# Kernel optimization log

Hardware: AMD Instinct MI355X
Metric: run time of the kernel (lower is better)

The kernel has to match this reference:

```python
import jax, jax.numpy as jnp
import numpy as np

C_IN = 256
GROUP = C_IN // 4  # module hard-codes group = C_in/4 -> 4 channels per group
EPS = 1e-5

@jax.custom_vjp
def binarize(x):
    # 1-bit quantization: sign forward, hardtanh straight-through backward
    return jnp.sign(x)

def _bin_fwd(x):
    return jnp.sign(x), x

def _bin_bwd(x, g):
    return (g * (jnp.abs(x) <= 1.0).astype(g.dtype),)

binarize.defvjp(_bin_fwd, _bin_bwd)

def channel_shuffle(x, g):
    # [N,C,H,W] -> [N,g,C/g,H,W] -> [N,C/g,g,H,W] -> [N,C,H,W]
    N, C, H, W = x.shape
    return x.reshape(N, g, C // g, H, W).transpose(0, 2, 1, 3, 4).reshape(N, C, H, W)


def setup_inputs() -> dict:
    key = jax.random.key(0)
    ks = jax.random.split(key, 6)
    x = jax.random.normal(ks[0], (32, C_IN, 56, 56), jnp.float32)
    # grouped conv weight: [C_out, C_in/group, kH, kW] = [256, 4, 3, 3]
    weight = jax.random.normal(ks[1], (C_IN, C_IN // GROUP, 3, 3), jnp.float32) * 0.1
    gamma = 1.0 + 0.1 * jax.random.normal(ks[2], (C_IN,), jnp.float32)
    beta = 0.1 * jax.random.normal(ks[3], (C_IN,), jnp.float32)
    running_mean = 0.1 * jax.random.normal(ks[4], (C_IN,), jnp.float32)
    running_var = jax.random.uniform(ks[5], (C_IN,), jnp.float32, 0.5, 1.5)
    return dict(x=x, weight=weight, gamma=gamma, beta=beta,
                running_mean=running_mean, running_var=running_var)


def reference(x, weight, gamma, beta, running_mean, running_var):
    # BatchNorm2d (inference-mode, affine=True)
    inv = gamma * jax.lax.rsqrt(running_var + EPS)
    xb = x * inv[None, :, None, None] + (beta - running_mean * inv)[None, :, None, None]
    # Conv2d_1w1a: binarize activations and weights, grouped 3x3 conv, no bias
    a = binarize(xb)
    w = binarize(weight)
    out = jax.lax.conv_general_dilated(
        a, w,
        window_strides=(1, 1),
        padding=((1, 1), (1, 1)),
        dimension_numbers=('NCHW', 'OIHW', 'NCHW'),
        feature_group_count=GROUP,
    )
    out = channel_shuffle(out, GROUP)
    # stride == 1 -> shortcut is identity
    return out + x
```

## Files before the change

### kernel.cpp

```cpp
#include <hip/hip_runtime.h>
#include <stdint.h>

#define H 56
#define W 56
#define HW (H * W)
#define CIN 256
#define IMG (CIN * HW)
#define EPS 1e-5f

#define ROWW 8
#define TROWS 58

__device__ __forceinline__ float mul_rn(float a, float b) {
    float d; asm("v_mul_f32 %0, %1, %2" : "=v"(d) : "v"(a), "v"(b)); return d;
}
__device__ __forceinline__ float add_rn(float a, float b) {
    float d; asm("v_add_f32 %0, %1, %2" : "=v"(d) : "v"(a), "v"(b)); return d;
}
__device__ __forceinline__ float sub_rn(float a, float b) {
    float d; asm("v_sub_f32 %0, %1, %2" : "=v"(d) : "v"(a), "v"(b)); return d;
}

__global__ __launch_bounds__(256)
void binconv_kernel(const float* __restrict__ X,
                    const float* __restrict__ Wt,
                    const float* __restrict__ gamma,
                    const float* __restrict__ beta,
                    const float* __restrict__ mean,
                    const float* __restrict__ var,
                    float* __restrict__ out) {
    __shared__ uint32_t s_tile[TROWS * ROWW];
    __shared__ uint32_t z_tile[TROWS * ROWW];
    __shared__ uint32_t ws_l[4][3];
    __shared__ uint32_t wz_l[4][3];

    const int bx  = blockIdx.x;
    const int n   = bx >> 6;
    const int g   = bx & 63;
    const int tid = threadIdx.x;

    for (int i = tid; i < TROWS * ROWW; i += 256) { s_tile[i] = 0u; z_tile[i] = 0u; }

    if (tid < 4) {
        const float* wc = Wt + (size_t)(g * 4 + tid) * 36;
        for (int r = 0; r < 3; ++r) {
            uint32_t s = 0, z = 0;
            for (int ci = 0; ci < 4; ++ci)
                for (int kw = 0; kw < 3; ++kw) {
                    float v = wc[ci * 9 + r * 3 + kw];
                    int b = kw * 4 + ci;
                    s |= (v > 0.f  ? 1u : 0u) << b;
                    z |= (v != 0.f ? 1u : 0u) << b;
                }
            ws_l[tid][r] = s; wz_l[tid][r] = z;
        }
    }

    float inv[4], bias[4];
#pragma unroll
    for (int ci = 0; ci < 4; ++ci) {
        int c = g * 4 + ci;
        float s  = sqrtf(var[c] + EPS);
        float r  = 1.0f / s;
        float iv = mul_rn(gamma[c], r);
        inv[ci]  = iv;
        bias[ci] = sub_rn(beta[c], mul_rn(mean[c], iv));
    }

    __syncthreads();

    const float* Xn = X + (size_t)n * IMG;

    for (int task = tid; task < 56 * 14; task += 256) {
        int r  = task / 14;
        int cg = task - r * 14;
        int off = r * W + cg * 4;
        uint32_t s16 = 0, z16 = 0;
#pragma unroll
        for (int ci = 0; ci < 4; ++ci) {
            const float4 v = *reinterpret_cast<const float4*>(
                Xn + (size_t)(g * 4 + ci) * HW + off);
            float t0 = add_rn(mul_rn(v.x, inv[ci]), bias[ci]);
            float t1 = add_rn(mul_rn(v.y, inv[ci]), bias[ci]);
            float t2 = add_rn(mul_rn(v.z, inv[ci]), bias[ci]);
            float t3 = add_rn(mul_rn(v.w, inv[ci]), bias[ci]);
            s16 |= ((t0 > 0.f ? 1u : 0u) << ci)        | ((t1 > 0.f ? 1u : 0u) << (4 + ci))
                 | ((t2 > 0.f ? 1u : 0u) << (8 + ci))  | ((t3 > 0.f ? 1u : 0u) << (12 + ci));
            z16 |= ((t0 != 0.f ? 1u : 0u) << ci)       | ((t1 != 0.f ? 1u : 0u) << (4 + ci))
                 | ((t2 != 0.f ? 1u : 0u) << (8 + ci)) | ((t3 != 0.f ? 1u : 0u) << (12 + ci));
        }
        reinterpret_cast<uint16_t*>(&s_tile[(r + 1) * ROWW])[cg] = (uint16_t)s16;
        reinterpret_cast<uint16_t*>(&z_tile[(r + 1) * ROWW])[cg] = (uint16_t)z16;
    }

    __syncthreads();

    uint32_t wsj[4][3], wzj[4][3];
    bool full = true;
#pragma unroll
    for (int j = 0; j < 4; ++j)
#pragma unroll
        for (int r = 0; r < 3; ++r) {
            wsj[j][r] = ws_l[j][r];
            wzj[j][r] = wz_l[j][r];
            full = full && (wzj[j][r] == 0xFFFu);
        }

    float* On = out + (size_t)n * IMG;

    for (int task = tid; task < 56 * 14; task += 256) {
        int h  = task / 14;
        int cg = task - h * 14;
        int w0 = cg * 4;

        uint64_t vs[3], vz[3];
        int off;
        if (w0 == 0) {
            off = 0;
#pragma unroll
            for (int r = 0; r < 3; ++r) {
                int base = (h + r) * ROWW;
                vs[r] = (((uint64_t)s_tile[base] | ((uint64_t)s_tile[base + 1] << 32)) << 4);
                vz[r] = (((uint64_t)z_tile[base] | ((uint64_t)z_tile[base + 1] << 32)) << 4);
            }
        } else {
            int st = 4 * w0 - 4;
            int i0 = st >> 5;
            off = st & 31;
#pragma unroll
            for (int r = 0; r < 3; ++r) {
                int base = (h + r) * ROWW + i0;
                vs[r] = ((uint64_t)s_tile[base] | ((uint64_t)s_tile[base + 1] << 32));
                vz[r] = ((uint64_t)z_tile[base] | ((uint64_t)z_tile[base + 1] << 32));
            }
        }

        int res[4][4];
        if (full) {
#pragma unroll
            for (int k = 0; k < 4; ++k) {
                int sh = off + 4 * k;
                uint32_t s0 = (uint32_t)(vs[0] >> sh) & 0xFFFu;
                uint32_t s1 = (uint32_t)(vs[1] >> sh) & 0xFFFu;
                uint32_t s2 = (uint32_t)(vs[2] >> sh) & 0xFFFu;
                uint32_t z0 = (uint32_t)(vz[0] >> sh) & 0xFFFu;
                uint32_t z1 = (uint32_t)(vz[1] >> sh) & 0xFFFu;
                uint32_t z2 = (uint32_t)(vz[2] >> sh) & 0xFFFu;
                int vb = __popc(z0) + __popc(z1) + __popc(z2);
#pragma unroll
                for (int j = 0; j < 4; ++j) {
                    int pc = __popc((s0 ^ wsj[j][0]) & z0)
                           + __popc((s1 ^ wsj[j][1]) & z1)
                           + __popc((s2 ^ wsj[j][2]) & z2);
                    res[j][k] = vb - 2 * pc;
                }
            }
        } else {
#pragma unroll
            for (int k = 0; k < 4; ++k) {
                int sh = off + 4 * k;
                uint32_t s0 = (uint32_t)(vs[0] >> sh) & 0xFFFu;
                uint32_t s1 = (uint32_t)(vs[1] >> sh) & 0xFFFu;
                uint32_t s2 = (uint32_t)(vs[2] >> sh) & 0xFFFu;
                uint32_t z0 = (uint32_t)(vz[0] >> sh) & 0xFFFu;
                uint32_t z1 = (uint32_t)(vz[1] >> sh) & 0xFFFu;
                uint32_t z2 = (uint32_t)(vz[2] >> sh) & 0xFFFu;
#pragma unroll
                for (int j = 0; j < 4; ++j) {
                    uint32_t m0 = z0 & wzj[j][0];
                    uint32_t m1 = z1 & wzj[j][1];
                    uint32_t m2 = z2 & wzj[j][2];
                    int vb = __popc(m0) + __popc(m1) + __popc(m2);
                    int pc = __popc((s0 ^ wsj[j][0]) & m0)
                           + __popc((s1 ^ wsj[j][1]) & m1)
                           + __popc((s2 ^ wsj[j][2]) & m2);
                    res[j][k] = vb - 2 * pc;
                }
            }
        }

        size_t pbase = (size_t)h * W + w0;
#pragma unroll
        for (int j = 0; j < 4; ++j) {
            size_t cofs = (size_t)(j * 64 + g) * HW + pbase;
            const float4 sc = *reinterpret_cast<const float4*>(Xn + cofs);
            float4 o;
            o.x = add_rn((float)res[j][0], sc.x);
            o.y = add_rn((float)res[j][1], sc.y);
            o.z = add_rn((float)res[j][2], sc.z);
            o.w = add_rn((float)res[j][3], sc.w);
            *reinterpret_cast<float4*>(On + cofs) = o;
        }
    }
}

extern "C" void kernel_launch(void* const* d_in, const int* in_sizes, int n_in,
                              void* d_out, int out_size, void* d_ws, size_t ws_size,
                              hipStream_t stream) {
    const float* X     = (const float*)d_in[0];
    const float* Wt    = (const float*)d_in[1];
    const float* gamma = (const float*)d_in[2];
    const float* beta  = (const float*)d_in[3];
    const float* mean  = (const float*)d_in[4];
    const float* var   = (const float*)d_in[5];
    float* out = (float*)d_out;

    int N = in_sizes[0] / IMG;

    binconv_kernel<<<N * 64, 256, 0, stream>>>(X, Wt, gamma, beta, mean, var, out);
}
```

Before: 205.1 us.

## Give each wavefront its own 14-row tile and drop block-wide barriers

Each 64-lane wavefront now handles a 14-row quarter of one image-group, with halo rows recomputed, instead of a 256-thread block covering the whole 56-row image. Weight bit patterns are built by 12 lanes and broadcast with shuffles rather than through shared memory, and __syncthreads is replaced by a wave-local lgkmcnt wait. This removes block barriers and serialization between the binarize and conv phases, at the cost of recomputing two halo rows per tile (16 vs 14 rows). It relies on intra-wavefront LDS visibility after the waitcnt.

```diff
diff --git a/kernel.cpp b/kernel.cpp
--- a/kernel.cpp
+++ b/kernel.cpp
@@ -9,7 +9,7 @@
 #define EPS 1e-5f
 
 #define ROWW 8
-#define TROWS 58
+#define WROWS 16
 
 __device__ __forceinline__ float mul_rn(float a, float b) {
     float d; asm("v_mul_f32 %0, %1, %2" : "=v"(d) : "v"(a), "v"(b)); return d;
@@ -29,32 +29,44 @@
                     const float* __restrict__ mean,
                     const float* __restrict__ var,
                     float* __restrict__ out) {
-    __shared__ uint32_t s_tile[TROWS * ROWW];
-    __shared__ uint32_t z_tile[TROWS * ROWW];
-    __shared__ uint32_t ws_l[4][3];
-    __shared__ uint32_t wz_l[4][3];
-
-    const int bx  = blockIdx.x;
-    const int n   = bx >> 6;
-    const int g   = bx & 63;
-    const int tid = threadIdx.x;
-
-    for (int i = tid; i < TROWS * ROWW; i += 256) { s_tile[i] = 0u; z_tile[i] = 0u; }
-
-    if (tid < 4) {
-        const float* wc = Wt + (size_t)(g * 4 + tid) * 36;
+    __shared__ uint32_t s_tiles[4][WROWS * ROWW];
+    __shared__ uint32_t z_tiles[4][WROWS * ROWW];
+
+    const int wid  = threadIdx.x >> 6;
+    const int lane = threadIdx.x & 63;
+    const int tile = blockIdx.x * 4 + wid;
+    const int q    = tile & 3;
+    const int g    = (tile >> 2) & 63;
+    const int n    = tile >> 8;
+    const int row0 = q * 14 - 1;
+
+    uint32_t* st = s_tiles[wid];
+    uint32_t* zt = z_tiles[wid];
+
+    uint32_t spat = 0, zpat = 0;
+    if (lane < 12) {
+        int j = lane / 3, r = lane - j * 3;
+        const float* wc = Wt + (size_t)(g * 4 + j) * 36;
+#pragma unroll
+        for (int ci = 0; ci < 4; ++ci)
+#pragma unroll
+            for (int kw = 0; kw < 3; ++kw) {
+                float v = wc[ci * 9 + r * 3 + kw];
+                int b = kw * 4 + ci;
+                spat |= (v > 0.f  ? 1u : 0u) << b;
+                zpat |= (v != 0.f ? 1u : 0u) << b;
+            }
+    }
+    uint32_t wsj[4][3], wzj[4][3];
+    bool full = true;
+#pragma unroll
+    for (int j = 0; j < 4; ++j)
+#pragma unroll
         for (int r = 0; r < 3; ++r) {
-            uint32_t s = 0, z = 0;
-            for (int ci = 0; ci < 4; ++ci)
-                for (int kw = 0; kw < 3; ++kw) {
-                    float v = wc[ci * 9 + r * 3 + kw];
-                    int b = kw * 4 + ci;
-                    s |= (v > 0.f  ? 1u : 0u) << b;
-                    z |= (v != 0.f ? 1u : 0u) << b;
-                }
-            ws_l[tid][r] = s; wz_l[tid][r] = z;
-        }
-    }
+            wsj[j][r] = __shfl(spat, j * 3 + r, 64);
+            wzj[j][r] = __shfl(zpat, j * 3 + r, 64);
+            full = full && (wzj[j][r] == 0xFFFu);
+        }
 
     float inv[4], bias[4];
 #pragma unroll
@@ -67,71 +79,63 @@
         bias[ci] = sub_rn(beta[c], mul_rn(mean[c], iv));
     }
 
-    __syncthreads();
+    if (lane < WROWS) { st[lane * ROWW + 7] = 0u; zt[lane * ROWW + 7] = 0u; }
 
     const float* Xn = X + (size_t)n * IMG;
 
-    for (int task = tid; task < 56 * 14; task += 256) {
-        int r  = task / 14;
-        int cg = task - r * 14;
-        int off = r * W + cg * 4;
+    for (int t = lane; t < WROWS * 14; t += 64) {
+        int r  = t / 14;
+        int cg = t - r * 14;
+        int gr = row0 + r;
         uint32_t s16 = 0, z16 = 0;
-#pragma unroll
-        for (int ci = 0; ci < 4; ++ci) {
-            const float4 v = *reinterpret_cast<const float4*>(
-                Xn + (size_t)(g * 4 + ci) * HW + off);
-            float t0 = add_rn(mul_rn(v.x, inv[ci]), bias[ci]);
-            float t1 = add_rn(mul_rn(v.y, inv[ci]), bias[ci]);
-            float t2 = add_rn(mul_rn(v.z, inv[ci]), bias[ci]);
-            float t3 = add_rn(mul_rn(v.w, inv[ci]), bias[ci]);
-            s16 |= ((t0 > 0.f ? 1u : 0u) << ci)        | ((t1 > 0.f ? 1u : 0u) << (4 + ci))
-                 | ((t2 > 0.f ? 1u : 0u) << (8 + ci))  | ((t3 > 0.f ? 1u : 0u) << (12 + ci));
+        if ((unsigned)gr < (unsigned)H) {
+            int off = gr * W + cg * 4;
+#pragma unroll
+            for (int ci = 0; ci < 4; ++ci) {
+                const float4 v = *reinterpret_cast<const float4*>(
+                    Xn + (size_t)(g * 4 + ci) * HW + off);
+                float t0 = add_rn(mul_rn(v.x, inv[ci]), bias[ci]);
+                float t1 = add_rn(mul_rn(v.y, inv[ci]), bias[ci]);
+                float t2 = add_rn(mul_rn(v.z, inv[ci]), bias[ci]);
+                float t3 = add_rn(mul_rn(v.w, inv[ci]), bias[ci]);
+                s16 |= ((t0 > 0.f ? 1u : 0u) << ci)        | ((t1 > 0.f ? 1u : 0u) << (4 + ci))
+                     | ((t2 > 0.f ? 1u : 0u) << (8 + ci))  | ((t3 > 0.f ? 1u : 0u) << (12 + ci));
             z16 |= ((t0 != 0.f ? 1u : 0u) << ci)       | ((t1 != 0.f ? 1u : 0u) << (4 + ci))
                  | ((t2 != 0.f ? 1u : 0u) << (8 + ci)) | ((t3 != 0.f ? 1u : 0u) << (12 + ci));
-        }
-        reinterpret_cast<uint16_t*>(&s_tile[(r + 1) * ROWW])[cg] = (uint16_t)s16;
-        reinterpret_cast<uint16_t*>(&z_tile[(r + 1) * ROWW])[cg] = (uint16_t)z16;
-    }
-
-    __syncthreads();
-
-    uint32_t wsj[4][3], wzj[4][3];
-    bool full = true;
-#pragma unroll
-    for (int j = 0; j < 4; ++j)
-#pragma unroll
-        for (int r = 0; r < 3; ++r) {
-            wsj[j][r] = ws_l[j][r];
-            wzj[j][r] = wz_l[j][r];
-            full = full && (wzj[j][r] == 0xFFFu);
-        }
+            }
+        }
+        reinterpret_cast<uint16_t*>(&st[r * ROWW])[cg] = (uint16_t)s16;
+        reinterpret_cast<uint16_t*>(&zt[r * ROWW])[cg] = (uint16_t)z16;
+    }
+
+    asm volatile("s_waitcnt lgkmcnt(0)" ::: "memory");
 
     float* On = out + (size_t)n * IMG;
 
-    for (int task = tid; task < 56 * 14; task += 256) {
-        int h  = task / 14;
-        int cg = task - h * 14;
+    for (int t = lane; t < 14 * 14; t += 64) {
+        int h  = t / 14;
+        int cg = t - h * 14;
         int w0 = cg * 4;
 
         uint64_t vs[3], vz[3];
         int off;
-        if (w0 == 0) {
+        if (cg == 0) {
             off = 0;
 #pragma unroll
             for (int r = 0; r < 3; ++r) {
                 int base = (h + r) * ROWW;
-                vs[r] = (((uint64_t)s_tile[base] | ((uint64_t)s_tile[base + 1] << 32)) << 4);
-                vz[r] = (((uint64_t)z_tile[base] | ((uint64_t)z_tile[base + 1] << 32)) << 4);
+                vs[r] = (((uint64_t)st[base] | ((uint64_t)st[base + 1] << 32)) << 4);
+                vz[r] = (((uint64_t)zt[base] | ((uint64_t)zt[base + 1] << 32)) << 4);
             }
         } else {
-            int st = 4 * w0 - 4;
-            int i0 = st >> 5;
-            off = st & 31;
+            int stb = 4 * w0 - 4;
+            int i0  = stb >> 5;
+            off     = stb & 31;
 #pragma unroll
             for (int r = 0; r < 3; ++r) {
                 int base = (h + r) * ROWW + i0;
-                vs[r] = ((uint64_t)s_tile[base] | ((uint64_t)s_tile[base + 1] << 32));
-                vz[r] = ((uint64_t)z_tile[base] | ((uint64_t)z_tile[base + 1] << 32));
+                vs[r] = ((uint64_t)st[base] | ((uint64_t)st[base + 1] << 32));
+                vz[r] = ((uint64_t)zt[base] | ((uint64_t)zt[base + 1] << 32));
             }
         }
 
@@ -179,7 +183,7 @@
             }
         }
 
-        size_t pbase = (size_t)h * W + w0;
+        size_t pbase = (size_t)(q * 14 + h) * W + w0;
 #pragma unroll
         for (int j = 0; j < 4; ++j) {
             size_t cofs = (size_t)(j * 64 + g) * HW + pbase;
```

Result: slower. 210.3 us (+2.5%).
